# Kernel optimization log

Hardware: AMD Instinct MI355X
Metric: run time of the kernel (lower is better)

## Reference

```python
import jax, jax.numpy as jnp
import numpy as np

N_HEADS = 16
N_KV_HEADS = 4
HEAD_DIM = 128


def apply_rope(x, cos, sin):
    # x: [b, h, s, head_dim]; cos/sin: [1, 1, s, head_dim//2]
    d = x.shape[-1] // 2
    x1, x2 = x[..., :d], x[..., d:]
    return jnp.concatenate([x1 * cos - x2 * sin, x1 * sin + x2 * cos], axis=-1)


def setup_inputs() -> dict:
    key = jax.random.key(0)
    ks = jax.random.split(key, 9)
    b, s, dim = 2, 2048, 2048
    inp = {
        "x": jax.random.normal(ks[0], (b, s, dim), jnp.float32),
        "cos": jax.random.normal(ks[1], (1, 1, s, HEAD_DIM // 2), jnp.float32),
        "sin": jax.random.normal(ks[2], (1, 1, s, HEAD_DIM // 2), jnp.float32),
        "Wq": jax.random.normal(ks[3], (dim, N_HEADS * HEAD_DIM), jnp.float32) * 0.02,
        "bq": jax.random.normal(ks[4], (N_HEADS * HEAD_DIM,), jnp.float32) * 0.02,
        "Wkv": jax.random.normal(ks[5], (dim, 2 * N_KV_HEADS * HEAD_DIM), jnp.float32) * 0.02,
        "bkv": jax.random.normal(ks[6], (2 * N_KV_HEADS * HEAD_DIM,), jnp.float32) * 0.02,
        "Wo": jax.random.normal(ks[7], (N_HEADS * HEAD_DIM, dim), jnp.float32) * 0.02,
        "bo": jax.random.normal(ks[8], (dim,), jnp.float32) * 0.02,
        "causal": 1,
    }
    return inp


def reference(x, cos, sin, Wq, bq, Wkv, bkv, Wo, bo, causal):
    b, s, dim = x.shape
    scale = 1.0 / np.sqrt(HEAD_DIM)
    # QKV projections (torch Linear with weight stored transposed here)
    q = (x @ Wq + bq).reshape(b, s, N_HEADS, HEAD_DIM).transpose(0, 2, 1, 3)
    kv = x @ Wkv + bkv  # [b, s, 2*n_kv*hd]
    k, v = jnp.split(kv, 2, axis=-1)
    k = k.reshape(b, s, N_KV_HEADS, HEAD_DIM).transpose(0, 2, 1, 3)
    v = v.reshape(b, s, N_KV_HEADS, HEAD_DIM).transpose(0, 2, 1, 3)
    q = apply_rope(q, cos, sin)
    k = apply_rope(k, cos, sin)
    # GQA: repeat kv heads
    rep = N_HEADS // N_KV_HEADS
    k = jnp.repeat(k, rep, axis=1)
    v = jnp.repeat(v, rep, axis=1)
    logits = jnp.einsum("bhqd,bhkd->bhqk", q, k) * scale
    if causal:
        mask = jnp.tril(jnp.ones((s, s), dtype=bool))
        logits = jnp.where(mask[None, None], logits, jnp.finfo(logits.dtype).min)
    scores = jax.nn.softmax(logits, axis=-1)
    vo = jnp.einsum("bhqk,bhkd->bhqd", scores, v)
    vo = vo.transpose(0, 2, 1, 3).reshape(b, s, N_HEADS * HEAD_DIM)
    out = vo @ Wo + bo
    return out
```

## Files before the change

kernel.cpp:

```cpp
#include <hip/hip_runtime.h>
#include <hip/hip_bf16.h>

typedef __bf16 bf16x8 __attribute__((ext_vector_type(8)));
typedef float  f32x4  __attribute__((ext_vector_type(4)));
typedef unsigned int u32;

#define GLD_LDS16(gp, lp) __builtin_amdgcn_global_load_lds( \
    (const __attribute__((address_space(1))) u32*)(gp), \
    (__attribute__((address_space(3))) u32*)(lp), 16, 0, 0)

template<int CTRL>
__device__ __forceinline__ float dpp_rot(float x) {
    int y = __builtin_amdgcn_update_dpp(__float_as_int(x), __float_as_int(x),
                                        CTRL, 0xF, 0xF, false);
    return __int_as_float(y);
}
__device__ __forceinline__ float rowmax16(float x) {
    x = fmaxf(x, dpp_rot<0x121>(x));
    x = fmaxf(x, dpp_rot<0x122>(x));
    x = fmaxf(x, dpp_rot<0x124>(x));
    x = fmaxf(x, dpp_rot<0x128>(x));
    return x;
}
__device__ __forceinline__ float rowsum16(float x) {
    x += dpp_rot<0x121>(x);
    x += dpp_rot<0x122>(x);
    x += dpp_rot<0x124>(x);
    x += dpp_rot<0x128>(x);
    return x;
}


__global__ __launch_bounds__(256) void f32_to_bf16_kernel(
    const float* __restrict__ in, __bf16* __restrict__ out, size_t n) {
    size_t i = ((size_t)blockIdx.x * 256 + threadIdx.x) * 8;
    if (i >= n) return;
    float4 a = *(const float4*)(in + i);
    float4 b = *(const float4*)(in + i + 4);
    bf16x8 v;
    v[0] = (__bf16)a.x; v[1] = (__bf16)a.y; v[2] = (__bf16)a.z; v[3] = (__bf16)a.w;
    v[4] = (__bf16)b.x; v[5] = (__bf16)b.y; v[6] = (__bf16)b.z; v[7] = (__bf16)b.w;
    *(bf16x8*)(out + i) = v;
}

__global__ __launch_bounds__(256) void transpose_to_bf16_kernel(
    const float* __restrict__ W, __bf16* __restrict__ Wt, int K, int N) {
    __shared__ float tile[32][33];
    int n0 = blockIdx.x * 32, k0 = blockIdx.y * 32;
    int tx = threadIdx.x, ty = threadIdx.y;
    #pragma unroll
    for (int i = 0; i < 32; i += 8)
        tile[ty + i][tx] = W[(size_t)(k0 + ty + i) * N + n0 + tx];
    __syncthreads();
    #pragma unroll
    for (int i = 0; i < 32; i += 8)
        Wt[(size_t)(n0 + ty + i) * K + k0 + tx] = (__bf16)tile[tx][ty + i];
}

__global__ __launch_bounds__(256) void concat_bias_kernel(
    const float* __restrict__ bq, const float* __restrict__ bkv,
    float* __restrict__ bqkv) {
    int i = blockIdx.x * 256 + threadIdx.x;
    if (i < 2048) bqkv[i] = bq[i];
    else if (i < 3072) bqkv[i] = bkv[i - 2048];
}

__global__ __launch_bounds__(256) void transpose_v_kernel(
    const __bf16* __restrict__ qkv, __bf16* __restrict__ vtg, int S) {
    __shared__ __bf16 tile[32][33];
    int s0 = blockIdx.x * 32, d0 = blockIdx.y * 32, z = blockIdx.z;
    int b = z >> 2, kvh = z & 3;
    int tx = threadIdx.x, ty = threadIdx.y;
    #pragma unroll
    for (int i = 0; i < 32; i += 8)
        tile[ty + i][tx] =
            qkv[((size_t)b * S + s0 + ty + i) * 3072 + 2560 + kvh * 128 + d0 + tx];
    __syncthreads();
    #pragma unroll
    for (int i = 0; i < 32; i += 8)
        vtg[((size_t)z * 128 + d0 + ty + i) * S + s0 + tx] = tile[tx][ty + i];
}

#define BM 128
#define BN 128
#define BK 64

template <typename OutT>
__global__ __launch_bounds__(256) void gemm_bt_bias_kernel(
    const __bf16* __restrict__ A, const __bf16* __restrict__ Bt,
    const float* __restrict__ bias, OutT* __restrict__ C,
    int M, int N, int K) {
    __shared__ __bf16 As[BM * BK];
    __shared__ __bf16 Bs[BN * BK];
    int tid  = threadIdx.x;
    int bm   = blockIdx.x;
    int bn   = blockIdx.y;
    int wave = tid >> 6;
    int lane = tid & 63;
    int wm   = (wave >> 1) * 64;
    int wn   = (wave & 1) * 64;
    int quad = lane >> 4;
    int l16  = lane & 15;
    int gr   = wave * 32 + (lane >> 3);
    int gc   = (lane & 7) * 8;

    f32x4 acc[4][4];
    f32x4 zero = {0.f, 0.f, 0.f, 0.f};
    #pragma unroll
    for (int i = 0; i < 4; ++i)
        #pragma unroll
        for (int j = 0; j < 4; ++j) acc[i][j] = zero;

    const __bf16* Abase = A  + (size_t)(bm * BM) * K;
    const __bf16* Bbase = Bt + (size_t)(bn * BN) * K;

    for (int k0 = 0; k0 < K; k0 += BK) {
        if (k0) __syncthreads();
        #pragma unroll
        for (int i = 0; i < 4; ++i) {
            GLD_LDS16(Abase + (size_t)(gr + i * 8) * K + k0 + gc,
                      &As[(wave * 32 + i * 8) * BK]);
            GLD_LDS16(Bbase + (size_t)(gr + i * 8) * K + k0 + gc,
                      &Bs[(wave * 32 + i * 8) * BK]);
        }
        __syncthreads();

        bf16x8 af[4][2], bf[4][2];
        #pragma unroll
        for (int i = 0; i < 4; ++i)
            #pragma unroll
            for (int kc = 0; kc < 2; ++kc)
                af[i][kc] = *(bf16x8*)&As[(wm + i * 16 + l16) * BK + kc * 32 + quad * 8];
        #pragma unroll
        for (int j = 0; j < 4; ++j)
            #pragma unroll
            for (int kc = 0; kc < 2; ++kc)
                bf[j][kc] = *(bf16x8*)&Bs[(wn + j * 16 + l16) * BK + kc * 32 + quad * 8];
        #pragma unroll
        for (int kc = 0; kc < 2; ++kc)
            #pragma unroll
            for (int i = 0; i < 4; ++i)
                #pragma unroll
                for (int j = 0; j < 4; ++j)
                    acc[i][j] = __builtin_amdgcn_mfma_f32_16x16x32_bf16(
                        af[i][kc], bf[j][kc], acc[i][j], 0, 0, 0);
    }

    #pragma unroll
    for (int i = 0; i < 4; ++i) {
        int row = bm * BM + wm + i * 16 + quad * 4;
        #pragma unroll
        for (int j = 0; j < 4; ++j) {
            int col  = bn * BN + wn + j * 16 + l16;
            float bv = bias[col];
            #pragma unroll
            for (int r = 0; r < 4; ++r)
                C[(size_t)(row + r) * N + col] = (OutT)(acc[i][j][r] + bv);
        }
    }
}

__global__ __launch_bounds__(256) void rope_kernel(
    __bf16* __restrict__ buf, const float* __restrict__ cosp,
    const float* __restrict__ sinp, int heads, int rowstride, int coloff,
    int S, int total) {
    int idx = blockIdx.x * 256 + threadIdx.x;
    if (idx >= total) return;
    int d  = idx & 63;
    int t2 = idx >> 6;
    int h  = t2 % heads;
    int r  = t2 / heads;
    int s  = r & (S - 1);
    size_t base = (size_t)r * rowstride + coloff + h * 128;
    float x1 = (float)buf[base + d];
    float x2 = (float)buf[base + d + 64];
    float c  = cosp[s * 64 + d];
    float sn = sinp[s * 64 + d];
    buf[base + d]      = (__bf16)(x1 * c - x2 * sn);
    buf[base + d + 64] = (__bf16)(x1 * sn + x2 * c);
}

#define PS_STR 72

__global__ __launch_bounds__(256, 2) void flash_mfma_kernel(
    const __bf16* __restrict__ qkv,
    const __bf16* __restrict__ vtg,
    __bf16* __restrict__ vo,
    const int* __restrict__ causal_p, int S) {
    __shared__ __bf16 Ks[2][64 * 128];
    __shared__ __bf16 Ps[4 * 16 * PS_STR];

    const int QKV = 3072;
    int tid  = threadIdx.x;
    int wave = tid >> 6;
    int lane = tid & 63;
    int quad = lane >> 4;
    int l16  = lane & 15;
    int id   = blockIdx.x;
    int xcd  = id & 7;
    int b    = xcd >> 2;
    int kvh  = xcd & 3;
    int rest = id >> 3;
    int hh   = rest & 3;
    int pair = rest >> 2;
    int h    = kvh * 4 + hh;
    int causal = causal_p[0];
    const float SCALE = 0.08838834764831845f;

    const __bf16* vB = vtg + ((size_t)(b * 4 + kvh) * 128) * S;

    #pragma unroll 1
    for (int phase = 0; phase < 2; ++phase) {
        int qt = phase ? (31 - pair) : pair;
        int q0 = qt * 64;
        int nt = causal ? (qt + 1) : (S / 64);

        bf16x8 a_frag[4];
        size_t qrow = ((size_t)b * S + q0 + wave * 16 + l16) * QKV + h * 128 + quad * 8;
        #pragma unroll
        for (int kc = 0; kc < 4; ++kc)
            a_frag[kc] = *(const bf16x8*)(qkv + qrow + kc * 32);

        f32x4 o_acc[8];
        f32x4 zero4 = {0.f, 0.f, 0.f, 0.f};
        #pragma unroll
        for (int dt = 0; dt < 8; ++dt) o_acc[dt] = zero4;
        float m_[4], l_[4];
        #pragma unroll
        for (int r = 0; r < 4; ++r) { m_[r] = -1e30f; l_[r] = 0.f; }
        int qrow_d = q0 + wave * 16 + quad * 4;

        __syncthreads();
        {
            size_t kg = ((size_t)b * S + wave * 16 + l16) * QKV + 2048 + kvh * 128 + quad * 8;
            #pragma unroll
            for (int kc = 0; kc < 4; ++kc)
                GLD_LDS16(qkv + kg + kc * 32, &Ks[0][(wave * 4 + kc) * 512]);
        }

        for (int t = 0; t < nt; ++t) {
            int cur = t & 1;
            __syncthreads();
            if (t + 1 < nt) {
                size_t kg = ((size_t)b * S + (t + 1) * 64 + wave * 16 + l16) * QKV
                            + 2048 + kvh * 128 + quad * 8;
                #pragma unroll
                for (int kc = 0; kc < 4; ++kc)
                    GLD_LDS16(qkv + kg + kc * 32, &Ks[1 - cur][(wave * 4 + kc) * 512]);
            }
            int j0 = t * 64;

            bf16x8 vf[8][2];
            #pragma unroll
            for (int dt = 0; dt < 8; ++dt) {
                const __bf16* vp = vB + (size_t)(dt * 16 + l16) * S + j0 + quad * 8;
                vf[dt][0] = *(const bf16x8*)(vp);
                vf[dt][1] = *(const bf16x8*)(vp + 32);
            }

            f32x4 s_t[4];
            #pragma unroll
            for (int jt = 0; jt < 4; ++jt) s_t[jt] = zero4;
            #pragma unroll
            for (int jt = 0; jt < 4; ++jt)
                #pragma unroll
                for (int kc = 0; kc < 4; ++kc) {
                    bf16x8 kf = *(bf16x8*)&Ks[cur][(jt * 4 + kc) * 512 + lane * 8];
                    s_t[jt] = __builtin_amdgcn_mfma_f32_16x16x32_bf16(
                        a_frag[kc], kf, s_t[jt], 0, 0, 0);
                }

            int diag = causal && (t == nt - 1);
            #pragma unroll
            for (int jt = 0; jt < 4; ++jt)
                #pragma unroll
                for (int r = 0; r < 4; ++r) {
                    float sv = s_t[jt][r] * SCALE;
                    if (diag && (j0 + jt * 16 + l16 > qrow_d + r)) sv = -1e30f;
                    s_t[jt][r] = sv;
                }

            float alpha[4];
            #pragma unroll
            for (int r = 0; r < 4; ++r) {
                float v = fmaxf(fmaxf(s_t[0][r], s_t[1][r]),
                                fmaxf(s_t[2][r], s_t[3][r]));
                v = rowmax16(v);
                float m_new = fmaxf(m_[r], v);
                alpha[r] = __expf(m_[r] - m_new);
                m_[r] = m_new;
                float rs = 0.f;
                #pragma unroll
                for (int jt = 0; jt < 4; ++jt) {
                    float p = __expf(s_t[jt][r] - m_new);
                    s_t[jt][r] = p;
                    rs += p;
                }
                l_[r] = l_[r] * alpha[r] + rs;
            }
            #pragma unroll
            for (int jt = 0; jt < 4; ++jt)
                #pragma unroll
                for (int r = 0; r < 4; ++r)
                    Ps[(wave * 16 + quad * 4 + r) * PS_STR + jt * 16 + l16] =
                        (__bf16)s_t[jt][r];
            #pragma unroll
            for (int dt = 0; dt < 8; ++dt)
                #pragma unroll
                for (int r = 0; r < 4; ++r) o_acc[dt][r] *= alpha[r];

            bf16x8 p0 = *(bf16x8*)&Ps[(wave * 16 + l16) * PS_STR + quad * 8];
            bf16x8 p1 = *(bf16x8*)&Ps[(wave * 16 + l16) * PS_STR + 32 + quad * 8];
            #pragma unroll
            for (int dt = 0; dt < 8; ++dt) {
                o_acc[dt] = __builtin_amdgcn_mfma_f32_16x16x32_bf16(
                    p0, vf[dt][0], o_acc[dt], 0, 0, 0);
                o_acc[dt] = __builtin_amdgcn_mfma_f32_16x16x32_bf16(
                    p1, vf[dt][1], o_acc[dt], 0, 0, 0);
            }
        }

        float invl[4];
        #pragma unroll
        for (int r = 0; r < 4; ++r) invl[r] = 1.f / rowsum16(l_[r]);
        size_t obase = ((size_t)b * S + q0 + wave * 16 + quad * 4) * 2048
                       + h * 128 + l16;
        #pragma unroll
        for (int dt = 0; dt < 8; ++dt)
            #pragma unroll
            for (int r = 0; r < 4; ++r)
                vo[obase + (size_t)r * 2048 + dt * 16] = (__bf16)(o_acc[dt][r] * invl[r]);
    }
}


extern "C" void kernel_launch(void* const* d_in, const int* in_sizes, int n_in,
                              void* d_out, int out_size, void* d_ws, size_t ws_size,
                              hipStream_t stream) {
    const float* x    = (const float*)d_in[0];
    const float* cosp = (const float*)d_in[1];
    const float* sinp = (const float*)d_in[2];
    const float* Wq   = (const float*)d_in[3];
    const float* bq   = (const float*)d_in[4];
    const float* Wkv  = (const float*)d_in[5];
    const float* bkv  = (const float*)d_in[6];
    const float* Wo   = (const float*)d_in[7];
    const float* bo   = (const float*)d_in[8];
    const int* causal = (const int*)d_in[9];
    float* out = (float*)d_out;

    const int B = 2, S = 2048;
    const int M = B * S;

    char* w = (char*)d_ws;
    __bf16* x16    = (__bf16*)w; w += (size_t)M * 2048 * 2;
    __bf16* Wqkvt  = (__bf16*)w; w += (size_t)3072 * 2048 * 2;
    __bf16* Wot    = (__bf16*)w; w += (size_t)2048 * 2048 * 2;
    float*  bqkv   = (float*)w;  w += (size_t)3072 * 4;
    __bf16* qkvbuf = (__bf16*)w; w += (size_t)M * 3072 * 2;
    __bf16* vobuf  = x16;
    __bf16* vtg    = Wqkvt;

    f32_to_bf16_kernel<<<(M * 2048) / (256 * 8), 256, 0, stream>>>(x, x16, (size_t)M * 2048);
    transpose_to_bf16_kernel<<<dim3(2048 / 32, 2048 / 32), dim3(32, 8), 0, stream>>>(Wq, Wqkvt, 2048, 2048);
    transpose_to_bf16_kernel<<<dim3(1024 / 32, 2048 / 32), dim3(32, 8), 0, stream>>>(Wkv, Wqkvt + (size_t)2048 * 2048, 2048, 1024);
    transpose_to_bf16_kernel<<<dim3(2048 / 32, 2048 / 32), dim3(32, 8), 0, stream>>>(Wo, Wot, 2048, 2048);
    concat_bias_kernel<<<12, 256, 0, stream>>>(bq, bkv, bqkv);
    gemm_bt_bias_kernel<__bf16><<<dim3(M / BM, 3072 / BN), 256, 0, stream>>>(x16, Wqkvt, bqkv, qkvbuf, M, 3072, 2048);
    {
        int totq = M * 16 * 64;
        rope_kernel<<<(totq + 255) / 256, 256, 0, stream>>>(qkvbuf, cosp, sinp, 16, 3072, 0, S, totq);
        int totk = M * 4 * 64;
        rope_kernel<<<(totk + 255) / 256, 256, 0, stream>>>(qkvbuf, cosp, sinp, 4, 3072, 2048, S, totk);
    }
    transpose_v_kernel<<<dim3(S / 32, 128 / 32, B * 4), dim3(32, 8), 0, stream>>>(qkvbuf, vtg, S);
    flash_mfma_kernel<<<dim3(512), 256, 0, stream>>>(qkvbuf, vtg, vobuf, causal, S);
    gemm_bt_bias_kernel<float><<<dim3(M / BM, 2048 / BN), 256, 0, stream>>>(vobuf, Wot, bo, out, M, 2048, 2048);
}
```

Before: 435.8 us.

## Widen flash-attention KV tile to 128 with swizzled P buffer and MFMA priority

Each inner-loop iteration now processes 128 keys instead of 64, halving the iteration count. That removes one barrier, one online-softmax rescale and one set of V loads per 64 keys. The P staging buffer drops the padded stride for an XOR-swizzled 256-byte row layout to avoid LDS bank conflicts, and s_setprio brackets the MFMA sections. The trade-offs: LDS use and register pressure roughly double, the launch_bounds minimum-occupancy hint is removed, and causal diagonal tiles may compute an extra fully masked 64-key half.

```diff
diff --git a/kernel.cpp b/kernel.cpp
--- a/kernel.cpp
+++ b/kernel.cpp
@@ -180,15 +180,14 @@
     buf[base + d + 64] = (__bf16)(x1 * sn + x2 * c);
 }
 
-#define PS_STR 72
-
-__global__ __launch_bounds__(256, 2) void flash_mfma_kernel(
+
+__global__ __launch_bounds__(256) void flash_mfma_kernel(
     const __bf16* __restrict__ qkv,
     const __bf16* __restrict__ vtg,
     __bf16* __restrict__ vo,
     const int* __restrict__ causal_p, int S) {
-    __shared__ __bf16 Ks[2][64 * 128];
-    __shared__ __bf16 Ps[4 * 16 * PS_STR];
+    __shared__ __bf16 Ks[2][128 * 128];
+    __shared__ __bf16 Ps[4 * 16 * 128];
 
     const int QKV = 3072;
     int tid  = threadIdx.x;
@@ -208,12 +207,14 @@
     const float SCALE = 0.08838834764831845f;
 
     const __bf16* vB = vtg + ((size_t)(b * 4 + kvh) * 128) * S;
+    char* psw = (char*)Ps + wave * 4096;
 
     #pragma unroll 1
     for (int phase = 0; phase < 2; ++phase) {
         int qt = phase ? (31 - pair) : pair;
         int q0 = qt * 64;
-        int nt = causal ? (qt + 1) : (S / 64);
+        int nt64 = causal ? (qt + 1) : (S / 64);
+        int nt   = (nt64 + 1) >> 1;
 
         bf16x8 a_frag[4];
         size_t qrow = ((size_t)b * S + q0 + wave * 16 + l16) * QKV + h * 128 + quad * 8;
@@ -234,45 +235,55 @@
         {
             size_t kg = ((size_t)b * S + wave * 16 + l16) * QKV + 2048 + kvh * 128 + quad * 8;
             #pragma unroll
-            for (int kc = 0; kc < 4; ++kc)
-                GLD_LDS16(qkv + kg + kc * 32, &Ks[0][(wave * 4 + kc) * 512]);
+            for (int hf = 0; hf < 2; ++hf)
+                #pragma unroll
+                for (int kc = 0; kc < 4; ++kc)
+                    GLD_LDS16(qkv + kg + (size_t)hf * 64 * QKV + kc * 32,
+                              &Ks[0][((wave + hf * 4) * 4 + kc) * 512]);
         }
 
+        #pragma unroll 1
         for (int t = 0; t < nt; ++t) {
             int cur = t & 1;
             __syncthreads();
             if (t + 1 < nt) {
-                size_t kg = ((size_t)b * S + (t + 1) * 64 + wave * 16 + l16) * QKV
+                size_t kg = ((size_t)b * S + (t + 1) * 128 + wave * 16 + l16) * QKV
                             + 2048 + kvh * 128 + quad * 8;
                 #pragma unroll
-                for (int kc = 0; kc < 4; ++kc)
-                    GLD_LDS16(qkv + kg + kc * 32, &Ks[1 - cur][(wave * 4 + kc) * 512]);
+                for (int hf = 0; hf < 2; ++hf)
+                    #pragma unroll
+                    for (int kc = 0; kc < 4; ++kc)
+                        GLD_LDS16(qkv + kg + (size_t)hf * 64 * QKV + kc * 32,
+                                  &Ks[1 - cur][((wave + hf * 4) * 4 + kc) * 512]);
             }
-            int j0 = t * 64;
-
-            bf16x8 vf[8][2];
+            int j0 = t * 128;
+
+            bf16x8 vf[8][4];
             #pragma unroll
             for (int dt = 0; dt < 8; ++dt) {
                 const __bf16* vp = vB + (size_t)(dt * 16 + l16) * S + j0 + quad * 8;
-                vf[dt][0] = *(const bf16x8*)(vp);
-                vf[dt][1] = *(const bf16x8*)(vp + 32);
+                #pragma unroll
+                for (int ks = 0; ks < 4; ++ks)
+                    vf[dt][ks] = *(const bf16x8*)(vp + ks * 32);
             }
 
-            f32x4 s_t[4];
-            #pragma unroll
-            for (int jt = 0; jt < 4; ++jt) s_t[jt] = zero4;
-            #pragma unroll
-            for (int jt = 0; jt < 4; ++jt)
+            f32x4 s_t[8];
+            #pragma unroll
+            for (int jt = 0; jt < 8; ++jt) s_t[jt] = zero4;
+            __builtin_amdgcn_s_setprio(1);
+            #pragma unroll
+            for (int jt = 0; jt < 8; ++jt)
                 #pragma unroll
                 for (int kc = 0; kc < 4; ++kc) {
                     bf16x8 kf = *(bf16x8*)&Ks[cur][(jt * 4 + kc) * 512 + lane * 8];
                     s_t[jt] = __builtin_amdgcn_mfma_f32_16x16x32_bf16(
                         a_frag[kc], kf, s_t[jt], 0, 0, 0);
                 }
+            __builtin_amdgcn_s_setprio(0);
 
             int diag = causal && (t == nt - 1);
             #pragma unroll
-            for (int jt = 0; jt < 4; ++jt)
+            for (int jt = 0; jt < 8; ++jt)
                 #pragma unroll
                 for (int r = 0; r < 4; ++r) {
                     float sv = s_t[jt][r] * SCALE;
@@ -283,15 +294,18 @@
             float alpha[4];
             #pragma unroll
             for (int r = 0; r < 4; ++r) {
-                float v = fmaxf(fmaxf(s_t[0][r], s_t[1][r]),
-                                fmaxf(s_t[2][r], s_t[3][r]));
+                float v01 = fmaxf(s_t[0][r], s_t[1][r]);
+                float v23 = fmaxf(s_t[2][r], s_t[3][r]);
+                float v45 = fmaxf(s_t[4][r], s_t[5][r]);
+                float v67 = fmaxf(s_t[6][r], s_t[7][r]);
+                float v = fmaxf(fmaxf(v01, v23), fmaxf(v45, v67));
                 v = rowmax16(v);
                 float m_new = fmaxf(m_[r], v);
                 alpha[r] = __expf(m_[r] - m_new);
                 m_[r] = m_new;
                 float rs = 0.f;
                 #pragma unroll
-                for (int jt = 0; jt < 4; ++jt) {
+                for (int jt = 0; jt < 8; ++jt) {
                     float p = __expf(s_t[jt][r] - m_new);
                     s_t[jt][r] = p;
                     rs += p;
@@ -299,25 +313,33 @@
                 l_[r] = l_[r] * alpha[r] + rs;
             }
             #pragma unroll
-            for (int jt = 0; jt < 4; ++jt)
-                #pragma unroll
-                for (int r = 0; r < 4; ++r)
-                    Ps[(wave * 16 + quad * 4 + r) * PS_STR + jt * 16 + l16] =
+            for (int jt = 0; jt < 8; ++jt)
+                #pragma unroll
+                for (int r = 0; r < 4; ++r) {
+                    int prow = quad * 4 + r;
+                    int inb  = (jt * 16 + l16) * 2;
+                    *(__bf16*)(psw + prow * 256 + (inb ^ ((prow & 7) << 4))) =
                         (__bf16)s_t[jt][r];
+                }
             #pragma unroll
             for (int dt = 0; dt < 8; ++dt)
                 #pragma unroll
                 for (int r = 0; r < 4; ++r) o_acc[dt][r] *= alpha[r];
 
-            bf16x8 p0 = *(bf16x8*)&Ps[(wave * 16 + l16) * PS_STR + quad * 8];
-            bf16x8 p1 = *(bf16x8*)&Ps[(wave * 16 + l16) * PS_STR + 32 + quad * 8];
-            #pragma unroll
-            for (int dt = 0; dt < 8; ++dt) {
-                o_acc[dt] = __builtin_amdgcn_mfma_f32_16x16x32_bf16(
-                    p0, vf[dt][0], o_acc[dt], 0, 0, 0);
-                o_acc[dt] = __builtin_amdgcn_mfma_f32_16x16x32_bf16(
-                    p1, vf[dt][1], o_acc[dt], 0, 0, 0);
-            }
+            int rb  = l16 * 256;
+            int swz = (l16 & 7) << 4;
+            bf16x8 pa[4];
+            #pragma unroll
+            for (int ks = 0; ks < 4; ++ks)
+                pa[ks] = *(bf16x8*)(psw + rb + ((ks * 64 + quad * 16) ^ swz));
+            __builtin_amdgcn_s_setprio(1);
+            #pragma unroll
+            for (int dt = 0; dt < 8; ++dt)
+                #pragma unroll
+                for (int ks = 0; ks < 4; ++ks)
+                    o_acc[dt] = __builtin_amdgcn_mfma_f32_16x16x32_bf16(
+                        pa[ks], vf[dt][ks], o_acc[dt], 0, 0, 0);
+            __builtin_amdgcn_s_setprio(0);
         }
 
         float invl[4];
```

After: 528.2 us. 1.21x slower.
